# Kernel tuning notes

Measured on AMD Instinct MI355X. Metric: run time of the kernel, lower is better.

The kernel has to match this reference:

```python
import jax, jax.numpy as jnp
import numpy as np

B, T, L, INPUT_DIM = 16, 128, 100, 100
EMB = 100
FEAT = INPUT_DIM + 3 * EMB          # 400
HID, OUT = 128, 50
RNN_IN = 2 * INPUT_DIM + 3 * L      # 500
VOCAB = 10000 + 2


def setup_inputs() -> dict:
    key = jax.random.key(0)
    ks = jax.random.split(key, 12)
    first = jax.random.normal(ks[0], (B, T, INPUT_DIM), jnp.float32)
    idx = jax.random.randint(ks[1], (B, T, 3 * L), 0, VOCAB).astype(jnp.float32)
    x = jnp.concatenate([first, idx], axis=2)  # [B,T,400]
    s = 0.05
    return {
        "x": x,
        "embed_nodes": jax.random.normal(ks[2], (VOCAB, EMB), jnp.float32) * s,
        "embed_paths": jax.random.normal(ks[3], (VOCAB, EMB), jnp.float32) * s,
        "W_t": jax.random.normal(ks[4], (FEAT, FEAT), jnp.float32) / np.sqrt(FEAT),
        "b_t": jnp.zeros((FEAT,), jnp.float32),
        "W_a": jax.random.normal(ks[5], (FEAT, 1), jnp.float32) / np.sqrt(FEAT),
        "b_a": jnp.zeros((1,), jnp.float32),
        "W_ih": jax.random.normal(ks[6], (4 * HID, RNN_IN), jnp.float32) / np.sqrt(RNN_IN),
        "W_hh": jax.random.normal(ks[7], (4 * HID, HID), jnp.float32) / np.sqrt(HID),
        "b_ih": jnp.zeros((4 * HID,), jnp.float32),
        "b_hh": jnp.zeros((4 * HID,), jnp.float32),
        "W_fc": jax.random.normal(ks[8], (HID, OUT), jnp.float32) / np.sqrt(HID),
        "b_fc": jnp.zeros((OUT,), jnp.float32),
    }


def _lstm(xs, W_ih, W_hh, b_ih, b_hh):
    # xs: [B,T,D] -> out [B,T,H]; PyTorch gate order i,f,g,o
    def step(carry, xt):
        h, c = carry
        g = xt @ W_ih.T + h @ W_hh.T + (b_ih + b_hh)  # [B,4H]
        i, f, gg, o = jnp.split(g, 4, axis=-1)
        c = jax.nn.sigmoid(f) * c + jax.nn.sigmoid(i) * jnp.tanh(gg)
        h = jax.nn.sigmoid(o) * jnp.tanh(c)
        return (h, c), h
    h0 = jnp.zeros((xs.shape[0], HID), xs.dtype)
    (_, _), hs = jax.lax.scan(step, (h0, h0), jnp.swapaxes(xs, 0, 1))
    return jnp.swapaxes(hs, 0, 1)


def reference(x, embed_nodes, embed_paths, W_t, b_t, W_a, b_a,
              W_ih, W_hh, b_ih, b_hh, W_fc, b_fc):
    first = x[:, :, :INPUT_DIM]                                   # [B,T,100]
    c2v = x[:, :, INPUT_DIM:INPUT_DIM + 3 * L].reshape(B, T, L, 3).astype(jnp.int32)
    s_emb = embed_nodes[c2v[..., 0]]                              # [B,T,L,100]
    e_emb = embed_nodes[c2v[..., 2]]
    p_emb = embed_paths[c2v[..., 1]]
    att_part = jnp.broadcast_to(first[:, :, None, :], (B, T, L, INPUT_DIM))
    full = jnp.concatenate([s_emb, e_emb, p_emb, att_part], axis=3)  # [B,T,L,400]
    # dropout skipped (deterministic reference == evaluating=True path)
    transformed = jnp.tanh(full @ W_t + b_t)
    ctx = transformed @ W_a + b_a                                 # [B,T,L,1]
    # faithful to nn.Softmax(dim=1): softmax over the sequence axis T
    attn = jax.nn.softmax(ctx, axis=1)
    code_vectors = jnp.sum(full * attn, axis=2)                   # [B,T,400]
    rnn_input = jnp.concatenate([first, code_vectors], axis=2)    # [B,T,500]
    out = _lstm(rnn_input, W_ih, W_hh, b_ih, b_hh)                # [B,T,128]
    return jax.nn.sigmoid(out @ W_fc + b_fc)                      # [B,T,50]
```

## Files before the change

kernel.cpp:

```cpp
#include <hip/hip_runtime.h>
#include <hip/hip_bf16.h>
#include <stdint.h>

#define B_     16
#define T_     128
#define L_     100
#define IN_    100
#define EMB_   100
#define FEAT_  400
#define HID_   128
#define OUT_   50
#define RNNIN_ 500
#define VOCAB_ 10002
#define BT_    2048
#define TBLK   157

#define S_T    (0.16f / 127.0f)
#define INVS_T (127.0f / 0.16f)
#define S_E    (0.30f / 127.0f)
#define INVS_E (127.0f / 0.30f)

typedef __attribute__((ext_vector_type(8))) short short8;
typedef __attribute__((ext_vector_type(4))) short short4v;
typedef __attribute__((ext_vector_type(4))) float f32x4;

__device__ __forceinline__ float lo2f(unsigned int u) {
    union { unsigned int i; float f; } v; v.i = u << 16; return v.f;
}
__device__ __forceinline__ float fast_tanh(float x) {
    x = fminf(15.f, fmaxf(-15.f, x));
    float e = __expf(2.f * x);
    return (e - 1.f) * __builtin_amdgcn_rcpf(e + 1.f);
}
__device__ __forceinline__ float sigm(float x) {
    x = fminf(30.f, fmaxf(-30.f, x));
    float e = __expf(-x);
    return __builtin_amdgcn_rcpf(1.f + e);
}
__device__ __forceinline__ signed char q8(float v, float invs) {
    float t = fminf(127.f, fmaxf(-127.f, v * invs));
    return (signed char)__float2int_rn(t);
}
__device__ __forceinline__ int sb(unsigned int u, int k) {
    return (int)(signed char)(u >> (8 * k));
}

__global__ __launch_bounds__(256) void casts_k(
    const float* __restrict__ EN, const float* __restrict__ EP,
    const float* __restrict__ x, const float* __restrict__ Wt,
    const float* __restrict__ Wih, const float* __restrict__ Whh,
    __hip_bfloat16* __restrict__ ENb, __hip_bfloat16* __restrict__ EPb,
    signed char* __restrict__ EN8, signed char* __restrict__ EP8,
    __hip_bfloat16* __restrict__ x_bf, __hip_bfloat16* __restrict__ WtT,
    __hip_bfloat16* __restrict__ Wih_bf, __hip_bfloat16* __restrict__ Whh_bf)
{
    int t0 = blockIdx.x * 256 + threadIdx.x;
    const int stride = 256 * 256;
    int n1 = VOCAB_ * 100;
    for (int i = t0; i < n1; i += stride) {
        float v = EN[i];
        ENb[i] = __float2bfloat16(v);
        EN8[i] = q8(v, INVS_E);
    }
    for (int i = t0; i < n1; i += stride) {
        float v = EP[i];
        EPb[i] = __float2bfloat16(v);
        EP8[i] = q8(v, INVS_E);
    }
    for (int i = t0; i < BT_ * 100; i += stride) {
        int bt = i / 100, d = i - bt * 100;
        x_bf[i] = __float2bfloat16(x[(size_t)bt * 400 + d]);
    }
    for (int i = t0; i < 4 * 400 * 128; i += stride) {
        int w = i / (400 * 128), rem = i - w * 400 * 128;
        int n = rem >> 7, k = rem & 127;
        WtT[i] = __float2bfloat16((k < 100) ? Wt[(size_t)(w * 100 + k) * 400 + n] : 0.f);
    }
    for (int i = t0; i < 512 * 512; i += stride) {
        int g = i >> 9, k = i & 511;
        Wih_bf[i] = __float2bfloat16((k < 500) ? Wih[(size_t)g * 500 + k] : 0.f);
    }
    for (int i = t0; i < 512 * 128; i += stride) Whh_bf[i] = __float2bfloat16(Whh[i]);
}

__device__ __forceinline__ void load_a100(const __hip_bfloat16* __restrict__ arow,
                                          int kg, short8 af[4])
{
    af[0] = *(const short8*)(arow + kg * 8);
    af[1] = *(const short8*)(arow + 32 + kg * 8);
    af[2] = *(const short8*)(arow + 64 + kg * 8);
    short8 z = {};
    af[3] = z;
    if (kg == 0) {
        short4v t = *(const short4v*)(arow + 96);
        af[3][0] = t[0]; af[3][1] = t[1]; af[3][2] = t[2]; af[3][3] = t[3];
    }
}

__global__ __launch_bounds__(256) void mm_k(
    const __hip_bfloat16* __restrict__ ENb, const __hip_bfloat16* __restrict__ EPb,
    const __hip_bfloat16* __restrict__ x_bf, const __hip_bfloat16* __restrict__ WtT,
    const float* __restrict__ btb,
    signed char* __restrict__ Es, signed char* __restrict__ Ee,
    signed char* __restrict__ Ep, float* __restrict__ q)
{
    int blk = blockIdx.x, tid = threadIdx.x;
    int wave = tid >> 6, lane = tid & 63;
    int cl = lane & 15, kg = lane >> 4;

    if (blk < 3 * TBLK) {
        int which = blk / TBLK, mb = blk - which * TBLK;
        const __hip_bfloat16* A = (which == 2) ? EPb : ENb;
        signed char* outp = (which == 0) ? Es : ((which == 1) ? Ee : Ep);
        int r0 = mb * 64 + wave * 16;
        int ra = r0 + cl; if (ra > VOCAB_ - 1) ra = VOCAB_ - 1;
        short8 af[4];
        load_a100(A + (size_t)ra * 100, kg, af);
        const __hip_bfloat16* Bp = WtT + (size_t)which * 400 * 128;
        for (int n0 = 0; n0 < 25; n0++) {
            const __hip_bfloat16* brow = Bp + (size_t)(n0 * 16 + cl) * 128 + kg * 8;
            f32x4 acc = (f32x4){0.f, 0.f, 0.f, 0.f};
            acc = __builtin_amdgcn_mfma_f32_16x16x32_bf16(af[0], *(const short8*)(brow), acc, 0, 0, 0);
            acc = __builtin_amdgcn_mfma_f32_16x16x32_bf16(af[1], *(const short8*)(brow + 32), acc, 0, 0, 0);
            acc = __builtin_amdgcn_mfma_f32_16x16x32_bf16(af[2], *(const short8*)(brow + 64), acc, 0, 0, 0);
            acc = __builtin_amdgcn_mfma_f32_16x16x32_bf16(af[3], *(const short8*)(brow + 96), acc, 0, 0, 0);
            int colj = n0 * 16 + cl;
#pragma unroll
            for (int r = 0; r < 4; r++) {
                int gr = r0 + kg * 4 + r;
                if (gr < VOCAB_)
                    outp[(size_t)gr * 400 + colj] = q8(acc[r], INVS_T);
            }
        }
    } else {
        int mb = blk - 3 * TBLK;
        int r0 = mb * 64 + wave * 16;
        short8 af[4];
        load_a100(x_bf + (size_t)(r0 + cl) * 100, kg, af);
        const __hip_bfloat16* Bp = WtT + (size_t)3 * 400 * 128;
        for (int n0 = 0; n0 < 25; n0++) {
            const __hip_bfloat16* brow = Bp + (size_t)(n0 * 16 + cl) * 128 + kg * 8;
            f32x4 acc = (f32x4){0.f, 0.f, 0.f, 0.f};
            acc = __builtin_amdgcn_mfma_f32_16x16x32_bf16(af[0], *(const short8*)(brow), acc, 0, 0, 0);
            acc = __builtin_amdgcn_mfma_f32_16x16x32_bf16(af[1], *(const short8*)(brow + 32), acc, 0, 0, 0);
            acc = __builtin_amdgcn_mfma_f32_16x16x32_bf16(af[2], *(const short8*)(brow + 64), acc, 0, 0, 0);
            acc = __builtin_amdgcn_mfma_f32_16x16x32_bf16(af[3], *(const short8*)(brow + 96), acc, 0, 0, 0);
            int colj = n0 * 16 + cl;
            float bb = btb[colj];
#pragma unroll
            for (int r = 0; r < 4; r++) {
                int gr = r0 + kg * 4 + r;
                q[(size_t)gr * 400 + colj] = acc[r] + bb;
            }
        }
    }
}

__global__ __launch_bounds__(256) void stage_a(
    const float* __restrict__ x,
    const signed char* __restrict__ Es8, const signed char* __restrict__ Ee8,
    const signed char* __restrict__ Ep8,
    const float* __restrict__ q, const float* __restrict__ Wa,
    float* __restrict__ ctx)
{
    __shared__ int idx_s[300];
    int bt = blockIdx.x, tid = threadIdx.x;
    const float* xr = x + (size_t)bt * 400 + 100;
    for (int i = tid; i < 300; i += 256) idx_s[i] = (int)xr[i];
    int lane = tid & 63, wave = tid >> 6;
    bool act = lane < 50;
    int j0 = lane * 8;
    float qv[8], wv[8];
    if (act) {
        float4 qa = *(const float4*)(q + (size_t)bt * 400 + j0);
        float4 qb = *(const float4*)(q + (size_t)bt * 400 + j0 + 4);
        float4 wa = *(const float4*)(Wa + j0);
        float4 wb = *(const float4*)(Wa + j0 + 4);
        qv[0]=qa.x; qv[1]=qa.y; qv[2]=qa.z; qv[3]=qa.w;
        qv[4]=qb.x; qv[5]=qb.y; qv[6]=qb.z; qv[7]=qb.w;
        wv[0]=wa.x; wv[1]=wa.y; wv[2]=wa.z; wv[3]=wa.w;
        wv[4]=wb.x; wv[5]=wb.y; wv[6]=wb.z; wv[7]=wb.w;
    } else {
#pragma unroll
        for (int jj = 0; jj < 8; jj++) { qv[jj] = 0.f; wv[jj] = 0.f; }
    }
    __syncthreads();
    for (int l = wave; l < 100; l += 4) {
        int i0 = idx_s[3 * l], i1 = idx_s[3 * l + 1], i2 = idx_s[3 * l + 2];
        float sum = 0.f;
        if (act) {
            uint2 a  = ((const uint2*)(Es8 + (size_t)i0 * 400))[lane];
            uint2 b  = ((const uint2*)(Ee8 + (size_t)i2 * 400))[lane];
            uint2 cc = ((const uint2*)(Ep8 + (size_t)i1 * 400))[lane];
            int zi[8];
#pragma unroll
            for (int k = 0; k < 4; k++) {
                zi[k]     = sb(a.x, k) + sb(b.x, k) + sb(cc.x, k);
                zi[4 + k] = sb(a.y, k) + sb(b.y, k) + sb(cc.y, k);
            }
#pragma unroll
            for (int jj = 0; jj < 8; jj++) {
                float z = fmaf((float)zi[jj], S_T, qv[jj]);
                sum = fmaf(fast_tanh(z), wv[jj], sum);
            }
        }
#pragma unroll
        for (int off = 32; off; off >>= 1) sum += __shfl_xor(sum, off);
        if (lane == 0) ctx[(size_t)bt * 100 + l] = sum;
    }
}

__global__ __launch_bounds__(256) void softmax_w(
    const float* __restrict__ ctx, float* __restrict__ attn)
{
    int wid = blockIdx.x * 4 + (threadIdx.x >> 6);
    int lane = threadIdx.x & 63;
    int b = wid / 100, l = wid - b * 100;
    size_t base = (size_t)b * 128 * 100 + l;
    float v0 = ctx[base + (size_t)lane * 100];
    float v1 = ctx[base + (size_t)(lane + 64) * 100];
    float m = fmaxf(v0, v1);
#pragma unroll
    for (int off = 32; off; off >>= 1) m = fmaxf(m, __shfl_xor(m, off));
    float e0 = __expf(v0 - m), e1 = __expf(v1 - m);
    float s = e0 + e1;
#pragma unroll
    for (int off = 32; off; off >>= 1) s += __shfl_xor(s, off);
    float rs = 1.f / s;
    attn[base + (size_t)lane * 100] = e0 * rs;
    attn[base + (size_t)(lane + 64) * 100] = e1 * rs;
}

__global__ __launch_bounds__(128) void stage_c(
    const float* __restrict__ x, const float* __restrict__ attn,
    const signed char* __restrict__ EN8, const signed char* __restrict__ EP8,
    __hip_bfloat16* __restrict__ rnn_bf)
{
    __shared__ float at[100];
    __shared__ int idx[300];
    int bt = blockIdx.x, tid = threadIdx.x;
    if (tid < 100) at[tid] = attn[(size_t)bt * 100 + tid];
    const float* xr = x + (size_t)bt * 400 + 100;
    for (int i = tid; i < 300; i += 128) idx[i] = (int)xr[i];
    __syncthreads();
    int d = tid;
    __hip_bfloat16* o = rnn_bf + (size_t)bt * 512;
    if (d < 100) {
        float as = 0.f, ae = 0.f, ap = 0.f, sa = 0.f;
#pragma unroll 4
        for (int l = 0; l < 100; l++) {
            float a = at[l]; sa += a;
            as = fmaf(a, (float)EN8[(size_t)idx[3 * l] * 100 + d], as);
            ae = fmaf(a, (float)EN8[(size_t)idx[3 * l + 2] * 100 + d], ae);
            ap = fmaf(a, (float)EP8[(size_t)idx[3 * l + 1] * 100 + d], ap);
        }
        float fi = x[(size_t)bt * 400 + d];
        o[d]       = __float2bfloat16(fi);
        o[100 + d] = __float2bfloat16(as * S_E);
        o[200 + d] = __float2bfloat16(ae * S_E);
        o[300 + d] = __float2bfloat16(ap * S_E);
        o[400 + d] = __float2bfloat16(fi * sa);
    } else if (d < 112) {
        o[400 + d] = __float2bfloat16(0.f);
    }
}

__global__ __launch_bounds__(256) void gemm_x(
    const __hip_bfloat16* __restrict__ rnn_bf, const __hip_bfloat16* __restrict__ Wih_bf,
    const float* __restrict__ bih, const float* __restrict__ bhh,
    float* __restrict__ X)
{
    int blk = blockIdx.x, tid = threadIdx.x;
    int wave = tid >> 6, lane = tid & 63;
    int cl = lane & 15, kg = lane >> 4;
    int r0 = blk * 64 + wave * 16;

    short8 af[16];
    const __hip_bfloat16* arow = rnn_bf + (size_t)(r0 + cl) * 512 + kg * 8;
#pragma unroll
    for (int ks = 0; ks < 16; ks++) af[ks] = *(const short8*)(arow + ks * 32);

    for (int n0 = 0; n0 < 32; n0 += 2) {
        const __hip_bfloat16* b0 = Wih_bf + (size_t)(n0 * 16 + cl) * 512 + kg * 8;
        const __hip_bfloat16* b1 = b0 + 16 * 512;
        f32x4 acA = (f32x4){0.f, 0.f, 0.f, 0.f};
        f32x4 acB = (f32x4){0.f, 0.f, 0.f, 0.f};
#pragma unroll
        for (int ks = 0; ks < 16; ks++) {
            acA = __builtin_amdgcn_mfma_f32_16x16x32_bf16(af[ks], *(const short8*)(b0 + ks * 32), acA, 0, 0, 0);
            acB = __builtin_amdgcn_mfma_f32_16x16x32_bf16(af[ks], *(const short8*)(b1 + ks * 32), acB, 0, 0, 0);
        }
        int c0 = n0 * 16 + cl, c1 = c0 + 16;
        float bi0 = bih[c0] + bhh[c0];
        float bi1 = bih[c1] + bhh[c1];
#pragma unroll
        for (int r = 0; r < 4; r++) {
            int m = r0 + kg * 4 + r;
            X[(size_t)m * 512 + c0] = acA[r] + bi0;
            X[(size_t)m * 512 + c1] = acB[r] + bi1;
        }
    }
}

__global__ __launch_bounds__(512, 1) void lstm_k(
    const float* __restrict__ X, const __hip_bfloat16* __restrict__ Whh_bf,
    float* __restrict__ hs)
{
    int b = blockIdx.x, tid = threadIdx.x;
    int wave = tid >> 6, lane = tid & 63;
    int col = lane & 15, kg = lane >> 4;

    short8 bf[4][4];
#pragma unroll
    for (int n = 0; n < 4; n++) {
        int g = n * 128 + wave * 16 + col;
#pragma unroll
        for (int kk = 0; kk < 4; kk++)
            bf[n][kk] = *(const short8*)(Whh_bf + (size_t)g * 128 + kk * 32 + kg * 8);
    }

    __shared__ __hip_bfloat16 hbuf[2][128];
    __shared__ float Xs[16][512];
    __shared__ float hsb_s[16][128];
    float c = 0.f;
    if (tid < 128) hbuf[0][tid] = __float2bfloat16(0.f);
    const float* xb = X + (size_t)b * 128 * 512;
    float* hb = hs + (size_t)b * 128 * 128;
    int j = wave * 16 + col;
    int p = 0;

    __syncthreads();

    for (int tc = 0; tc < 8; tc++) {
        {
            const float* src = xb + (size_t)tc * 16 * 512 + tid;
#pragma unroll
            for (int k = 0; k < 16; k++) Xs[k][tid] = src[k * 512];
        }
        __syncthreads();

#pragma unroll 1
        for (int ts = 0; ts < 16; ts++) {
            short8 af[4];
            short8 zz = {};
#pragma unroll
            for (int kk = 0; kk < 4; kk++) {
                af[kk] = zz;
                if (col == 0) af[kk] = *(const short8*)(&hbuf[p][0] + kk * 32 + kg * 8);
            }
            f32x4 acc[4];
#pragma unroll
            for (int n = 0; n < 4; n++) acc[n] = (f32x4){0.f, 0.f, 0.f, 0.f};
#pragma unroll
            for (int kk = 0; kk < 4; kk++)
#pragma unroll
                for (int n = 0; n < 4; n++)
                    acc[n] = __builtin_amdgcn_mfma_f32_16x16x32_bf16(af[kk], bf[n][kk], acc[n], 0, 0, 0);

            if (lane < 16) {
                float pi = acc[0][0] + Xs[ts][j];
                float pf = acc[1][0] + Xs[ts][128 + j];
                float pg = acc[2][0] + Xs[ts][256 + j];
                float po = acc[3][0] + Xs[ts][384 + j];
                c = sigm(pf) * c + sigm(pi) * fast_tanh(pg);
                float hn = sigm(po) * fast_tanh(c);
                hbuf[p ^ 1][j] = __float2bfloat16(hn);
                hsb_s[ts][j] = hn;
            }
            __syncthreads();
            p ^= 1;
        }

        {
            float* dst = hb + (size_t)tc * 16 * 128;
#pragma unroll
            for (int k = 0; k < 4; k++) {
                int i = k * 512 + tid;
                dst[i] = hsb_s[i >> 7][i & 127];
            }
        }
    }
}

__global__ __launch_bounds__(64) void fc_k(
    const float* __restrict__ hs, const float* __restrict__ Wfc,
    const float* __restrict__ bfc, float* __restrict__ out)
{
    int r0 = blockIdx.x * 4, o = threadIdx.x;
    if (o >= 50) return;
    float acc[4] = {0.f, 0.f, 0.f, 0.f};
    for (int j = 0; j < 128; j++) {
        float wv = Wfc[j * 50 + o];
#pragma unroll
        for (int r = 0; r < 4; r++)
            acc[r] = fmaf(hs[(size_t)(r0 + r) * 128 + j], wv, acc[r]);
    }
    float bb = bfc[o];
#pragma unroll
    for (int r = 0; r < 4; r++) out[(size_t)(r0 + r) * 50 + o] = sigm(acc[r] + bb);
}

extern "C" void kernel_launch(void* const* d_in, const int* in_sizes, int n_in,
                              void* d_out, int out_size, void* d_ws, size_t ws_size,
                              hipStream_t stream) {
    const float* x   = (const float*)d_in[0];
    const float* EN  = (const float*)d_in[1];
    const float* EP  = (const float*)d_in[2];
    const float* Wt  = (const float*)d_in[3];
    const float* bt  = (const float*)d_in[4];
    const float* Wa  = (const float*)d_in[5];
    const float* Wih = (const float*)d_in[7];
    const float* Whh = (const float*)d_in[8];
    const float* bih = (const float*)d_in[9];
    const float* bhh = (const float*)d_in[10];
    const float* Wfc = (const float*)d_in[11];
    const float* bfc = (const float*)d_in[12];
    float* out = (float*)d_out;

    char* ws = (char*)d_ws;
    size_t off = 0;
    auto alloc = [&](size_t bytes) -> char* {
        char* p = ws + off;
        off = (off + bytes + 255) & ~(size_t)255;
        return p;
    };
    signed char* Es  = (signed char*)alloc((size_t)VOCAB_ * 400);
    signed char* Ee  = (signed char*)alloc((size_t)VOCAB_ * 400);
    signed char* Epb = (signed char*)alloc((size_t)VOCAB_ * 400);
    __hip_bfloat16* ENb    = (__hip_bfloat16*)alloc((size_t)VOCAB_ * 100 * 2);
    __hip_bfloat16* EPb    = (__hip_bfloat16*)alloc((size_t)VOCAB_ * 100 * 2);
    signed char* EN8 = (signed char*)alloc((size_t)VOCAB_ * 100);
    signed char* EP8 = (signed char*)alloc((size_t)VOCAB_ * 100);
    __hip_bfloat16* x_bf   = (__hip_bfloat16*)alloc((size_t)BT_ * 100 * 2);
    __hip_bfloat16* WtT    = (__hip_bfloat16*)alloc((size_t)4 * 400 * 128 * 2);
    __hip_bfloat16* Wih_bf = (__hip_bfloat16*)alloc((size_t)512 * 512 * 2);
    __hip_bfloat16* Whh_bf = (__hip_bfloat16*)alloc((size_t)512 * 128 * 2);
    __hip_bfloat16* rnn_bf = (__hip_bfloat16*)alloc((size_t)BT_ * 512 * 2);
    float* q    = (float*)alloc((size_t)BT_ * 400 * 4);
    float* ctx  = (float*)alloc((size_t)BT_ * 100 * 4);
    float* attn = (float*)alloc((size_t)BT_ * 100 * 4);
    float* X    = (float*)alloc((size_t)BT_ * 512 * 4);
    float* hsb  = (float*)alloc((size_t)BT_ * 128 * 4);

    casts_k<<<256, 256, 0, stream>>>(EN, EP, x, Wt, Wih, Whh,
                                     ENb, EPb, EN8, EP8, x_bf, WtT, Wih_bf, Whh_bf);
    mm_k<<<3 * TBLK + 32, 256, 0, stream>>>(ENb, EPb, x_bf, WtT, bt,
                                            Es, Ee, Epb, q);

    stage_a<<<BT_, 256, 0, stream>>>(x, Es, Ee, Epb, q, Wa, ctx);
    softmax_w<<<400, 256, 0, stream>>>(ctx, attn);
    stage_c<<<BT_, 128, 0, stream>>>(x, attn, EN8, EP8, rnn_bf);
    gemm_x<<<32, 256, 0, stream>>>(rnn_bf, Wih_bf, bih, bhh, X);
    lstm_k<<<B_, 512, 0, stream>>>(X, Whh_bf, hsb);
    fc_k<<<BT_ / 4, 64, 0, stream>>>(hsb, Wfc, bfc, out);
}
```

Measured before the change: 272.7 us.

## Fuse six pre-LSTM kernels into one persistent kernel with grid barriers

Merges the cast, embedding GEMM, attention-score, softmax, context-sum and input-projection kernels into a single persistent kernel of 512 blocks. The stages are separated by a software grid barrier built on atomics, which removes five kernel launches and the gaps between them. In exchange, stages with little work leave most blocks idle at each barrier. The barrier also assumes all 512 blocks are resident at once, and it needs an extra memset before each launch.

```diff
diff --git a/kernel.cpp b/kernel.cpp
--- a/kernel.cpp
+++ b/kernel.cpp
@@ -14,6 +14,7 @@
 #define VOCAB_ 10002
 #define BT_    2048
 #define TBLK   157
+#define GRID_  512
 
 #define S_T    (0.16f / 127.0f)
 #define INVS_T (127.0f / 0.16f)
@@ -24,9 +25,6 @@
 typedef __attribute__((ext_vector_type(4))) short short4v;
 typedef __attribute__((ext_vector_type(4))) float f32x4;
 
-__device__ __forceinline__ float lo2f(unsigned int u) {
-    union { unsigned int i; float f; } v; v.i = u << 16; return v.f;
-}
 __device__ __forceinline__ float fast_tanh(float x) {
     x = fminf(15.f, fmaxf(-15.f, x));
     float e = __expf(2.f * x);
@@ -45,42 +43,32 @@
     return (int)(signed char)(u >> (8 * k));
 }
 
-__global__ __launch_bounds__(256) void casts_k(
-    const float* __restrict__ EN, const float* __restrict__ EP,
-    const float* __restrict__ x, const float* __restrict__ Wt,
-    const float* __restrict__ Wih, const float* __restrict__ Whh,
-    __hip_bfloat16* __restrict__ ENb, __hip_bfloat16* __restrict__ EPb,
-    signed char* __restrict__ EN8, signed char* __restrict__ EP8,
-    __hip_bfloat16* __restrict__ x_bf, __hip_bfloat16* __restrict__ WtT,
-    __hip_bfloat16* __restrict__ Wih_bf, __hip_bfloat16* __restrict__ Whh_bf)
-{
-    int t0 = blockIdx.x * 256 + threadIdx.x;
-    const int stride = 256 * 256;
-    int n1 = VOCAB_ * 100;
-    for (int i = t0; i < n1; i += stride) {
-        float v = EN[i];
-        ENb[i] = __float2bfloat16(v);
-        EN8[i] = q8(v, INVS_E);
-    }
-    for (int i = t0; i < n1; i += stride) {
-        float v = EP[i];
-        EPb[i] = __float2bfloat16(v);
-        EP8[i] = q8(v, INVS_E);
-    }
-    for (int i = t0; i < BT_ * 100; i += stride) {
-        int bt = i / 100, d = i - bt * 100;
-        x_bf[i] = __float2bfloat16(x[(size_t)bt * 400 + d]);
-    }
-    for (int i = t0; i < 4 * 400 * 128; i += stride) {
-        int w = i / (400 * 128), rem = i - w * 400 * 128;
-        int n = rem >> 7, k = rem & 127;
-        WtT[i] = __float2bfloat16((k < 100) ? Wt[(size_t)(w * 100 + k) * 400 + n] : 0.f);
-    }
-    for (int i = t0; i < 512 * 512; i += stride) {
-        int g = i >> 9, k = i & 511;
-        Wih_bf[i] = __float2bfloat16((k < 500) ? Wih[(size_t)g * 500 + k] : 0.f);
-    }
-    for (int i = t0; i < 512 * 128; i += stride) Whh_bf[i] = __float2bfloat16(Whh[i]);
+struct Params {
+    const float *x, *EN, *EP, *Wt, *btb, *Wa, *Wih, *Whh, *bih, *bhh;
+    signed char *Es, *Ee, *Ep, *EN8, *EP8;
+    __hip_bfloat16 *ENb, *EPb, *x_bf, *WtT, *Wih_bf, *Whh_bf, *rnn_bf;
+    float *q, *ctx, *attn, *X;
+    unsigned *bar;
+};
+
+__device__ __forceinline__ void gbar(unsigned* bar, unsigned target) {
+    __syncthreads();
+    __threadfence();
+    if (threadIdx.x == 0) {
+        unsigned old = __hip_atomic_fetch_add(&bar[0], 1u, __ATOMIC_ACQ_REL,
+                                              __HIP_MEMORY_SCOPE_AGENT);
+        if (old == GRID_ - 1) {
+            __hip_atomic_store(&bar[0], 0u, __ATOMIC_RELAXED, __HIP_MEMORY_SCOPE_AGENT);
+            __hip_atomic_fetch_add(&bar[1], 1u, __ATOMIC_RELEASE,
+                                   __HIP_MEMORY_SCOPE_AGENT);
+        } else {
+            while (__hip_atomic_load(&bar[1], __ATOMIC_ACQUIRE,
+                                     __HIP_MEMORY_SCOPE_AGENT) < target)
+                __builtin_amdgcn_s_sleep(2);
+        }
+    }
+    __syncthreads();
+    __threadfence();
 }
 
 __device__ __forceinline__ void load_a100(const __hip_bfloat16* __restrict__ arow,
@@ -97,207 +85,220 @@
     }
 }
 
-__global__ __launch_bounds__(256) void mm_k(
-    const __hip_bfloat16* __restrict__ ENb, const __hip_bfloat16* __restrict__ EPb,
-    const __hip_bfloat16* __restrict__ x_bf, const __hip_bfloat16* __restrict__ WtT,
-    const float* __restrict__ btb,
-    signed char* __restrict__ Es, signed char* __restrict__ Ee,
-    signed char* __restrict__ Ep, float* __restrict__ q)
+__global__ __launch_bounds__(256, 2) void fused_k(Params p)
 {
-    int blk = blockIdx.x, tid = threadIdx.x;
-    int wave = tid >> 6, lane = tid & 63;
+    int bid = blockIdx.x, tid = threadIdx.x;
+    int lane = tid & 63, wave = tid >> 6;
     int cl = lane & 15, kg = lane >> 4;
 
-    if (blk < 3 * TBLK) {
-        int which = blk / TBLK, mb = blk - which * TBLK;
-        const __hip_bfloat16* A = (which == 2) ? EPb : ENb;
-        signed char* outp = (which == 0) ? Es : ((which == 1) ? Ee : Ep);
-        int r0 = mb * 64 + wave * 16;
-        int ra = r0 + cl; if (ra > VOCAB_ - 1) ra = VOCAB_ - 1;
-        short8 af[4];
-        load_a100(A + (size_t)ra * 100, kg, af);
-        const __hip_bfloat16* Bp = WtT + (size_t)which * 400 * 128;
-        for (int n0 = 0; n0 < 25; n0++) {
-            const __hip_bfloat16* brow = Bp + (size_t)(n0 * 16 + cl) * 128 + kg * 8;
-            f32x4 acc = (f32x4){0.f, 0.f, 0.f, 0.f};
-            acc = __builtin_amdgcn_mfma_f32_16x16x32_bf16(af[0], *(const short8*)(brow), acc, 0, 0, 0);
-            acc = __builtin_amdgcn_mfma_f32_16x16x32_bf16(af[1], *(const short8*)(brow + 32), acc, 0, 0, 0);
-            acc = __builtin_amdgcn_mfma_f32_16x16x32_bf16(af[2], *(const short8*)(brow + 64), acc, 0, 0, 0);
-            acc = __builtin_amdgcn_mfma_f32_16x16x32_bf16(af[3], *(const short8*)(brow + 96), acc, 0, 0, 0);
-            int colj = n0 * 16 + cl;
+    __shared__ int idx_s[300];
+    __shared__ float at2[2][100];
+    __shared__ int idx2[2][300];
+
+    {
+        int t0 = bid * 256 + tid;
+        const int stride = GRID_ * 256;
+        int n1 = VOCAB_ * 100;
+        for (int i = t0; i < n1; i += stride) {
+            float v = p.EN[i];
+            p.ENb[i] = __float2bfloat16(v);
+            p.EN8[i] = q8(v, INVS_E);
+        }
+        for (int i = t0; i < n1; i += stride) {
+            float v = p.EP[i];
+            p.EPb[i] = __float2bfloat16(v);
+            p.EP8[i] = q8(v, INVS_E);
+        }
+        for (int i = t0; i < BT_ * 100; i += stride) {
+            int bt = i / 100, d = i - bt * 100;
+            p.x_bf[i] = __float2bfloat16(p.x[(size_t)bt * 400 + d]);
+        }
+        for (int i = t0; i < 4 * 400 * 128; i += stride) {
+            int w = i / (400 * 128), rem = i - w * 400 * 128;
+            int n = rem >> 7, k = rem & 127;
+            p.WtT[i] = __float2bfloat16((k < 100) ? p.Wt[(size_t)(w * 100 + k) * 400 + n] : 0.f);
+        }
+        for (int i = t0; i < 512 * 512; i += stride) {
+            int g = i >> 9, k = i & 511;
+            p.Wih_bf[i] = __float2bfloat16((k < 500) ? p.Wih[(size_t)g * 500 + k] : 0.f);
+        }
+        for (int i = t0; i < 512 * 128; i += stride)
+            p.Whh_bf[i] = __float2bfloat16(p.Whh[i]);
+    }
+    gbar(p.bar, 1);
+
+    if (bid < 3 * TBLK + 32) {
+        if (bid < 3 * TBLK) {
+            int which = bid / TBLK, mb = bid - which * TBLK;
+            const __hip_bfloat16* A = (which == 2) ? p.EPb : p.ENb;
+            signed char* outp = (which == 0) ? p.Es : ((which == 1) ? p.Ee : p.Ep);
+            int r0 = mb * 64 + wave * 16;
+            int ra = r0 + cl; if (ra > VOCAB_ - 1) ra = VOCAB_ - 1;
+            short8 af[4];
+            load_a100(A + (size_t)ra * 100, kg, af);
+            const __hip_bfloat16* Bp = p.WtT + (size_t)which * 400 * 128;
+            for (int n0 = 0; n0 < 25; n0++) {
+                const __hip_bfloat16* brow = Bp + (size_t)(n0 * 16 + cl) * 128 + kg * 8;
+                f32x4 acc = (f32x4){0.f, 0.f, 0.f, 0.f};
+                acc = __builtin_amdgcn_mfma_f32_16x16x32_bf16(af[0], *(const short8*)(brow), acc, 0, 0, 0);
+                acc = __builtin_amdgcn_mfma_f32_16x16x32_bf16(af[1], *(const short8*)(brow + 32), acc, 0, 0, 0);
+                acc = __builtin_amdgcn_mfma_f32_16x16x32_bf16(af[2], *(const short8*)(brow + 64), acc, 0, 0, 0);
+                acc = __builtin_amdgcn_mfma_f32_16x16x32_bf16(af[3], *(const short8*)(brow + 96), acc, 0, 0, 0);
+                int colj = n0 * 16 + cl;
+#pragma unroll
+                for (int r = 0; r < 4; r++) {
+                    int gr = r0 + kg * 4 + r;
+                    if (gr < VOCAB_)
+                        outp[(size_t)gr * 400 + colj] = q8(acc[r], INVS_T);
+                }
+            }
+        } else {
+            int mb = bid - 3 * TBLK;
+            int r0 = mb * 64 + wave * 16;
+            short8 af[4];
+            load_a100(p.x_bf + (size_t)(r0 + cl) * 100, kg, af);
+            const __hip_bfloat16* Bp = p.WtT + (size_t)3 * 400 * 128;
+            for (int n0 = 0; n0 < 25; n0++) {
+                const __hip_bfloat16* brow = Bp + (size_t)(n0 * 16 + cl) * 128 + kg * 8;
+                f32x4 acc = (f32x4){0.f, 0.f, 0.f, 0.f};
+                acc = __builtin_amdgcn_mfma_f32_16x16x32_bf16(af[0], *(const short8*)(brow), acc, 0, 0, 0);
+                acc = __builtin_amdgcn_mfma_f32_16x16x32_bf16(af[1], *(const short8*)(brow + 32), acc, 0, 0, 0);
+                acc = __builtin_amdgcn_mfma_f32_16x16x32_bf16(af[2], *(const short8*)(brow + 64), acc, 0, 0, 0);
+                acc = __builtin_amdgcn_mfma_f32_16x16x32_bf16(af[3], *(const short8*)(brow + 96), acc, 0, 0, 0);
+                int colj = n0 * 16 + cl;
+                float bb = p.btb[colj];
+#pragma unroll
+                for (int r = 0; r < 4; r++) {
+                    int gr = r0 + kg * 4 + r;
+                    p.q[(size_t)gr * 400 + colj] = acc[r] + bb;
+                }
+            }
+        }
+    }
+    gbar(p.bar, 2);
+
+    for (int bt = bid; bt < BT_; bt += GRID_) {
+        const float* xr = p.x + (size_t)bt * 400 + 100;
+        for (int i = tid; i < 300; i += 256) idx_s[i] = (int)xr[i];
+        bool act = lane < 50;
+        int j0 = lane * 8;
+        float qv[8], wv[8];
+        if (act) {
+            float4 qa = *(const float4*)(p.q + (size_t)bt * 400 + j0);
+            float4 qb = *(const float4*)(p.q + (size_t)bt * 400 + j0 + 4);
+            float4 wa = *(const float4*)(p.Wa + j0);
+            float4 wb = *(const float4*)(p.Wa + j0 + 4);
+            qv[0]=qa.x; qv[1]=qa.y; qv[2]=qa.z; qv[3]=qa.w;
+            qv[4]=qb.x; qv[5]=qb.y; qv[6]=qb.z; qv[7]=qb.w;
+            wv[0]=wa.x; wv[1]=wa.y; wv[2]=wa.z; wv[3]=wa.w;
+            wv[4]=wb.x; wv[5]=wb.y; wv[6]=wb.z; wv[7]=wb.w;
+        } else {
+#pragma unroll
+            for (int jj = 0; jj < 8; jj++) { qv[jj] = 0.f; wv[jj] = 0.f; }
+        }
+        __syncthreads();
+        for (int l = wave; l < 100; l += 4) {
+            int i0 = idx_s[3 * l], i1 = idx_s[3 * l + 1], i2 = idx_s[3 * l + 2];
+            float sum = 0.f;
+            if (act) {
+                uint2 a  = ((const uint2*)(p.Es + (size_t)i0 * 400))[lane];
+                uint2 b  = ((const uint2*)(p.Ee + (size_t)i2 * 400))[lane];
+                uint2 cc = ((const uint2*)(p.Ep + (size_t)i1 * 400))[lane];
+                int zi[8];
+#pragma unroll
+                for (int k = 0; k < 4; k++) {
+                    zi[k]     = sb(a.x, k) + sb(b.x, k) + sb(cc.x, k);
+                    zi[4 + k] = sb(a.y, k) + sb(b.y, k) + sb(cc.y, k);
+                }
+#pragma unroll
+                for (int jj = 0; jj < 8; jj++) {
+                    float z = fmaf((float)zi[jj], S_T, qv[jj]);
+                    sum = fmaf(fast_tanh(z), wv[jj], sum);
+                }
+            }
+#pragma unroll
+            for (int off = 32; off; off >>= 1) sum += __shfl_xor(sum, off);
+            if (lane == 0) p.ctx[(size_t)bt * 100 + l] = sum;
+        }
+        __syncthreads();
+    }
+    gbar(p.bar, 3);
+
+    if (bid < 400) {
+        int wid = bid * 4 + wave;
+        int b = wid / 100, l = wid - b * 100;
+        size_t base = (size_t)b * 128 * 100 + l;
+        float v0 = p.ctx[base + (size_t)lane * 100];
+        float v1 = p.ctx[base + (size_t)(lane + 64) * 100];
+        float m = fmaxf(v0, v1);
+#pragma unroll
+        for (int off = 32; off; off >>= 1) m = fmaxf(m, __shfl_xor(m, off));
+        float e0 = __expf(v0 - m), e1 = __expf(v1 - m);
+        float s = e0 + e1;
+#pragma unroll
+        for (int off = 32; off; off >>= 1) s += __shfl_xor(s, off);
+        float rs = 1.f / s;
+        p.attn[base + (size_t)lane * 100] = e0 * rs;
+        p.attn[base + (size_t)(lane + 64) * 100] = e1 * rs;
+    }
+    gbar(p.bar, 4);
+
+    for (int role = bid; role < BT_ / 2; role += GRID_) {
+        int sub = tid >> 7, t1 = tid & 127;
+        int bt = role * 2 + sub;
+        if (t1 < 100) at2[sub][t1] = p.attn[(size_t)bt * 100 + t1];
+        const float* xr = p.x + (size_t)bt * 400 + 100;
+        for (int i = t1; i < 300; i += 128) idx2[sub][i] = (int)xr[i];
+        __syncthreads();
+        int d = t1;
+        __hip_bfloat16* o = p.rnn_bf + (size_t)bt * 512;
+        if (d < 100) {
+            float as = 0.f, ae = 0.f, ap = 0.f, sa = 0.f;
+#pragma unroll 4
+            for (int l = 0; l < 100; l++) {
+                float a = at2[sub][l]; sa += a;
+                as = fmaf(a, (float)p.EN8[(size_t)idx2[sub][3 * l] * 100 + d], as);
+                ae = fmaf(a, (float)p.EN8[(size_t)idx2[sub][3 * l + 2] * 100 + d], ae);
+                ap = fmaf(a, (float)p.EP8[(size_t)idx2[sub][3 * l + 1] * 100 + d], ap);
+            }
+            float fi = p.x[(size_t)bt * 400 + d];
+            o[d]       = __float2bfloat16(fi);
+            o[100 + d] = __float2bfloat16(as * S_E);
+            o[200 + d] = __float2bfloat16(ae * S_E);
+            o[300 + d] = __float2bfloat16(ap * S_E);
+            o[400 + d] = __float2bfloat16(fi * sa);
+        } else if (d < 112) {
+            o[400 + d] = __float2bfloat16(0.f);
+        }
+        __syncthreads();
+    }
+    gbar(p.bar, 5);
+
+    if (bid < 32) {
+        int r0 = bid * 64 + wave * 16;
+        short8 af[16];
+        const __hip_bfloat16* arow = p.rnn_bf + (size_t)(r0 + cl) * 512 + kg * 8;
+#pragma unroll
+        for (int ks = 0; ks < 16; ks++) af[ks] = *(const short8*)(arow + ks * 32);
+        for (int n0 = 0; n0 < 32; n0 += 2) {
+            const __hip_bfloat16* b0 = p.Wih_bf + (size_t)(n0 * 16 + cl) * 512 + kg * 8;
+            const __hip_bfloat16* b1 = b0 + 16 * 512;
+            f32x4 acA = (f32x4){0.f, 0.f, 0.f, 0.f};
+            f32x4 acB = (f32x4){0.f, 0.f, 0.f, 0.f};
+#pragma unroll
+            for (int ks = 0; ks < 16; ks++) {
+                acA = __builtin_amdgcn_mfma_f32_16x16x32_bf16(af[ks], *(const short8*)(b0 + ks * 32), acA, 0, 0, 0);
+                acB = __builtin_amdgcn_mfma_f32_16x16x32_bf16(af[ks], *(const short8*)(b1 + ks * 32), acB, 0, 0, 0);
+            }
+            int c0 = n0 * 16 + cl, c1 = c0 + 16;
+            float bi0 = p.bih[c0] + p.bhh[c0];
+            float bi1 = p.bih[c1] + p.bhh[c1];
 #pragma unroll
             for (int r = 0; r < 4; r++) {
-                int gr = r0 + kg * 4 + r;
-                if (gr < VOCAB_)
-                    outp[(size_t)gr * 400 + colj] = q8(acc[r], INVS_T);
-            }
-        }
-    } else {
-        int mb = blk - 3 * TBLK;
-        int r0 = mb * 64 + wave * 16;
-        short8 af[4];
-        load_a100(x_bf + (size_t)(r0 + cl) * 100, kg, af);
-        const __hip_bfloat16* Bp = WtT + (size_t)3 * 400 * 128;
-        for (int n0 = 0; n0 < 25; n0++) {
-            const __hip_bfloat16* brow = Bp + (size_t)(n0 * 16 + cl) * 128 + kg * 8;
-            f32x4 acc = (f32x4){0.f, 0.f, 0.f, 0.f};
-            acc = __builtin_amdgcn_mfma_f32_16x16x32_bf16(af[0], *(const short8*)(brow), acc, 0, 0, 0);
-            acc = __builtin_amdgcn_mfma_f32_16x16x32_bf16(af[1], *(const short8*)(brow + 32), acc, 0, 0, 0);
-            acc = __builtin_amdgcn_mfma_f32_16x16x32_bf16(af[2], *(const short8*)(brow + 64), acc, 0, 0, 0);
-            acc = __builtin_amdgcn_mfma_f32_16x16x32_bf16(af[3], *(const short8*)(brow + 96), acc, 0, 0, 0);
-            int colj = n0 * 16 + cl;
-            float bb = btb[colj];
-#pragma unroll
-            for (int r = 0; r < 4; r++) {
-                int gr = r0 + kg * 4 + r;
-                q[(size_t)gr * 400 + colj] = acc[r] + bb;
-            }
-        }
-    }
-}
-
-__global__ __launch_bounds__(256) void stage_a(
-    const float* __restrict__ x,
-    const signed char* __restrict__ Es8, const signed char* __restrict__ Ee8,
-    const signed char* __restrict__ Ep8,
-    const float* __restrict__ q, const float* __restrict__ Wa,
-    float* __restrict__ ctx)
-{
-    __shared__ int idx_s[300];
-    int bt = blockIdx.x, tid = threadIdx.x;
-    const float* xr = x + (size_t)bt * 400 + 100;
-    for (int i = tid; i < 300; i += 256) idx_s[i] = (int)xr[i];
-    int lane = tid & 63, wave = tid >> 6;
-    bool act = lane < 50;
-    int j0 = lane * 8;
-    float qv[8], wv[8];
-    if (act) {
-        float4 qa = *(const float4*)(q + (size_t)bt * 400 + j0);
-        float4 qb = *(const float4*)(q + (size_t)bt * 400 + j0 + 4);
-        float4 wa = *(const float4*)(Wa + j0);
-        float4 wb = *(const float4*)(Wa + j0 + 4);
-        qv[0]=qa.x; qv[1]=qa.y; qv[2]=qa.z; qv[3]=qa.w;
-        qv[4]=qb.x; qv[5]=qb.y; qv[6]=qb.z; qv[7]=qb.w;
-        wv[0]=wa.x; wv[1]=wa.y; wv[2]=wa.z; wv[3]=wa.w;
-        wv[4]=wb.x; wv[5]=wb.y; wv[6]=wb.z; wv[7]=wb.w;
-    } else {
-#pragma unroll
-        for (int jj = 0; jj < 8; jj++) { qv[jj] = 0.f; wv[jj] = 0.f; }
-    }
-    __syncthreads();
-    for (int l = wave; l < 100; l += 4) {
-        int i0 = idx_s[3 * l], i1 = idx_s[3 * l + 1], i2 = idx_s[3 * l + 2];
-        float sum = 0.f;
-        if (act) {
-            uint2 a  = ((const uint2*)(Es8 + (size_t)i0 * 400))[lane];
-            uint2 b  = ((const uint2*)(Ee8 + (size_t)i2 * 400))[lane];
-            uint2 cc = ((const uint2*)(Ep8 + (size_t)i1 * 400))[lane];
-            int zi[8];
-#pragma unroll
-            for (int k = 0; k < 4; k++) {
-                zi[k]     = sb(a.x, k) + sb(b.x, k) + sb(cc.x, k);
-                zi[4 + k] = sb(a.y, k) + sb(b.y, k) + sb(cc.y, k);
-            }
-#pragma unroll
-            for (int jj = 0; jj < 8; jj++) {
-                float z = fmaf((float)zi[jj], S_T, qv[jj]);
-                sum = fmaf(fast_tanh(z), wv[jj], sum);
-            }
-        }
-#pragma unroll
-        for (int off = 32; off; off >>= 1) sum += __shfl_xor(sum, off);
-        if (lane == 0) ctx[(size_t)bt * 100 + l] = sum;
-    }
-}
-
-__global__ __launch_bounds__(256) void softmax_w(
-    const float* __restrict__ ctx, float* __restrict__ attn)
-{
-    int wid = blockIdx.x * 4 + (threadIdx.x >> 6);
-    int lane = threadIdx.x & 63;
-    int b = wid / 100, l = wid - b * 100;
-    size_t base = (size_t)b * 128 * 100 + l;
-    float v0 = ctx[base + (size_t)lane * 100];
-    float v1 = ctx[base + (size_t)(lane + 64) * 100];
-    float m = fmaxf(v0, v1);
-#pragma unroll
-    for (int off = 32; off; off >>= 1) m = fmaxf(m, __shfl_xor(m, off));
-    float e0 = __expf(v0 - m), e1 = __expf(v1 - m);
-    float s = e0 + e1;
-#pragma unroll
-    for (int off = 32; off; off >>= 1) s += __shfl_xor(s, off);
-    float rs = 1.f / s;
-    attn[base + (size_t)lane * 100] = e0 * rs;
-    attn[base + (size_t)(lane + 64) * 100] = e1 * rs;
-}
-
-__global__ __launch_bounds__(128) void stage_c(
-    const float* __restrict__ x, const float* __restrict__ attn,
-    const signed char* __restrict__ EN8, const signed char* __restrict__ EP8,
-    __hip_bfloat16* __restrict__ rnn_bf)
-{
-    __shared__ float at[100];
-    __shared__ int idx[300];
-    int bt = blockIdx.x, tid = threadIdx.x;
-    if (tid < 100) at[tid] = attn[(size_t)bt * 100 + tid];
-    const float* xr = x + (size_t)bt * 400 + 100;
-    for (int i = tid; i < 300; i += 128) idx[i] = (int)xr[i];
-    __syncthreads();
-    int d = tid;
-    __hip_bfloat16* o = rnn_bf + (size_t)bt * 512;
-    if (d < 100) {
-        float as = 0.f, ae = 0.f, ap = 0.f, sa = 0.f;
-#pragma unroll 4
-        for (int l = 0; l < 100; l++) {
-            float a = at[l]; sa += a;
-            as = fmaf(a, (float)EN8[(size_t)idx[3 * l] * 100 + d], as);
-            ae = fmaf(a, (float)EN8[(size_t)idx[3 * l + 2] * 100 + d], ae);
-            ap = fmaf(a, (float)EP8[(size_t)idx[3 * l + 1] * 100 + d], ap);
-        }
-        float fi = x[(size_t)bt * 400 + d];
-        o[d]       = __float2bfloat16(fi);
-        o[100 + d] = __float2bfloat16(as * S_E);
-        o[200 + d] = __float2bfloat16(ae * S_E);
-        o[300 + d] = __float2bfloat16(ap * S_E);
-        o[400 + d] = __float2bfloat16(fi * sa);
-    } else if (d < 112) {
-        o[400 + d] = __float2bfloat16(0.f);
-    }
-}
-
-__global__ __launch_bounds__(256) void gemm_x(
-    const __hip_bfloat16* __restrict__ rnn_bf, const __hip_bfloat16* __restrict__ Wih_bf,
-    const float* __restrict__ bih, const float* __restrict__ bhh,
-    float* __restrict__ X)
-{
-    int blk = blockIdx.x, tid = threadIdx.x;
-    int wave = tid >> 6, lane = tid & 63;
-    int cl = lane & 15, kg = lane >> 4;
-    int r0 = blk * 64 + wave * 16;
-
-    short8 af[16];
-    const __hip_bfloat16* arow = rnn_bf + (size_t)(r0 + cl) * 512 + kg * 8;
-#pragma unroll
-    for (int ks = 0; ks < 16; ks++) af[ks] = *(const short8*)(arow + ks * 32);
-
-    for (int n0 = 0; n0 < 32; n0 += 2) {
-        const __hip_bfloat16* b0 = Wih_bf + (size_t)(n0 * 16 + cl) * 512 + kg * 8;
-        const __hip_bfloat16* b1 = b0 + 16 * 512;
-        f32x4 acA = (f32x4){0.f, 0.f, 0.f, 0.f};
-        f32x4 acB = (f32x4){0.f, 0.f, 0.f, 0.f};
-#pragma unroll
-        for (int ks = 0; ks < 16; ks++) {
-            acA = __builtin_amdgcn_mfma_f32_16x16x32_bf16(af[ks], *(const short8*)(b0 + ks * 32), acA, 0, 0, 0);
-            acB = __builtin_amdgcn_mfma_f32_16x16x32_bf16(af[ks], *(const short8*)(b1 + ks * 32), acB, 0, 0, 0);
-        }
-        int c0 = n0 * 16 + cl, c1 = c0 + 16;
-        float bi0 = bih[c0] + bhh[c0];
-        float bi1 = bih[c1] + bhh[c1];
-#pragma unroll
-        for (int r = 0; r < 4; r++) {
-            int m = r0 + kg * 4 + r;
-            X[(size_t)m * 512 + c0] = acA[r] + bi0;
-            X[(size_t)m * 512 + c1] = acB[r] + bi1;
+                int m = r0 + kg * 4 + r;
+                p.X[(size_t)m * 512 + c0] = acA[r] + bi0;
+                p.X[(size_t)m * 512 + c1] = acB[r] + bi1;
+            }
         }
     }
 }
@@ -424,6 +425,7 @@
         off = (off + bytes + 255) & ~(size_t)255;
         return p;
     };
+    unsigned* bar = (unsigned*)alloc(256);
     signed char* Es  = (signed char*)alloc((size_t)VOCAB_ * 400);
     signed char* Ee  = (signed char*)alloc((size_t)VOCAB_ * 400);
     signed char* Epb = (signed char*)alloc((size_t)VOCAB_ * 400);
@@ -442,15 +444,18 @@
     float* X    = (float*)alloc((size_t)BT_ * 512 * 4);
     float* hsb  = (float*)alloc((size_t)BT_ * 128 * 4);
 
-    casts_k<<<256, 256, 0, stream>>>(EN, EP, x, Wt, Wih, Whh,
-                                     ENb, EPb, EN8, EP8, x_bf, WtT, Wih_bf, Whh_bf);
-    mm_k<<<3 * TBLK + 32, 256, 0, stream>>>(ENb, EPb, x_bf, WtT, bt,
-                                            Es, Ee, Epb, q);
-
-    stage_a<<<BT_, 256, 0, stream>>>(x, Es, Ee, Epb, q, Wa, ctx);
-    softmax_w<<<400, 256, 0, stream>>>(ctx, attn);
-    stage_c<<<BT_, 128, 0, stream>>>(x, attn, EN8, EP8, rnn_bf);
-    gemm_x<<<32, 256, 0, stream>>>(rnn_bf, Wih_bf, bih, bhh, X);
+    hipMemsetAsync(bar, 0, 256, stream);
+
+    Params p;
+    p.x = x; p.EN = EN; p.EP = EP; p.Wt = Wt; p.btb = bt; p.Wa = Wa;
+    p.Wih = Wih; p.Whh = Whh; p.bih = bih; p.bhh = bhh;
+    p.Es = Es; p.Ee = Ee; p.Ep = Epb; p.EN8 = EN8; p.EP8 = EP8;
+    p.ENb = ENb; p.EPb = EPb; p.x_bf = x_bf; p.WtT = WtT;
+    p.Wih_bf = Wih_bf; p.Whh_bf = Whh_bf; p.rnn_bf = rnn_bf;
+    p.q = q; p.ctx = ctx; p.attn = attn; p.X = X;
+    p.bar = bar;
+
+    fused_k<<<GRID_, 256, 0, stream>>>(p);
     lstm_k<<<B_, 512, 0, stream>>>(X, Whh_bf, hsb);
     fc_k<<<BT_ / 4, 64, 0, stream>>>(hsb, Wfc, bfc, out);
 }
```

Measured after the change: 949.3 us. 3.48x slower.

## Fuse bf16 casts into embedding GEMM loads and fold input GEMM into LSTM

Applied to the files above, without the earlier changes.

The embedding and x bf16 copies are dropped, and mm_k now converts fp32 rows to bf16 in registers while loading its A fragments. The separate gemm_x launch is folded into lstm_k, so each batch block first computes its own 128x512 input projection before the recurrence. casts_k gets more blocks and handles less work. This removes two intermediate buffers and one kernel launch. In exchange the input GEMM runs on only 16 blocks instead of 32, and its result must be visible within the block before the recurrence reads X.

```diff
diff --git a/kernel.cpp b/kernel.cpp
--- a/kernel.cpp
+++ b/kernel.cpp
@@ -21,12 +21,8 @@
 #define INVS_E (127.0f / 0.30f)
 
 typedef __attribute__((ext_vector_type(8))) short short8;
-typedef __attribute__((ext_vector_type(4))) short short4v;
 typedef __attribute__((ext_vector_type(4))) float f32x4;
 
-__device__ __forceinline__ float lo2f(unsigned int u) {
-    union { unsigned int i; float f; } v; v.i = u << 16; return v.f;
-}
 __device__ __forceinline__ float fast_tanh(float x) {
     x = fminf(15.f, fmaxf(-15.f, x));
     float e = __expf(2.f * x);
@@ -47,30 +43,17 @@
 
 __global__ __launch_bounds__(256) void casts_k(
     const float* __restrict__ EN, const float* __restrict__ EP,
-    const float* __restrict__ x, const float* __restrict__ Wt,
-    const float* __restrict__ Wih, const float* __restrict__ Whh,
-    __hip_bfloat16* __restrict__ ENb, __hip_bfloat16* __restrict__ EPb,
+    const float* __restrict__ Wt, const float* __restrict__ Wih,
+    const float* __restrict__ Whh,
     signed char* __restrict__ EN8, signed char* __restrict__ EP8,
-    __hip_bfloat16* __restrict__ x_bf, __hip_bfloat16* __restrict__ WtT,
-    __hip_bfloat16* __restrict__ Wih_bf, __hip_bfloat16* __restrict__ Whh_bf)
+    __hip_bfloat16* __restrict__ WtT, __hip_bfloat16* __restrict__ Wih_bf,
+    __hip_bfloat16* __restrict__ Whh_bf)
 {
     int t0 = blockIdx.x * 256 + threadIdx.x;
-    const int stride = 256 * 256;
+    const int stride = 1024 * 256;
     int n1 = VOCAB_ * 100;
-    for (int i = t0; i < n1; i += stride) {
-        float v = EN[i];
-        ENb[i] = __float2bfloat16(v);
-        EN8[i] = q8(v, INVS_E);
-    }
-    for (int i = t0; i < n1; i += stride) {
-        float v = EP[i];
-        EPb[i] = __float2bfloat16(v);
-        EP8[i] = q8(v, INVS_E);
-    }
-    for (int i = t0; i < BT_ * 100; i += stride) {
-        int bt = i / 100, d = i - bt * 100;
-        x_bf[i] = __float2bfloat16(x[(size_t)bt * 400 + d]);
-    }
+    for (int i = t0; i < n1; i += stride) EN8[i] = q8(EN[i], INVS_E);
+    for (int i = t0; i < n1; i += stride) EP8[i] = q8(EP[i], INVS_E);
     for (int i = t0; i < 4 * 400 * 128; i += stride) {
         int w = i / (400 * 128), rem = i - w * 400 * 128;
         int n = rem >> 7, k = rem & 127;
@@ -83,23 +66,28 @@
     for (int i = t0; i < 512 * 128; i += stride) Whh_bf[i] = __float2bfloat16(Whh[i]);
 }
 
-__device__ __forceinline__ void load_a100(const __hip_bfloat16* __restrict__ arow,
-                                          int kg, short8 af[4])
-{
-    af[0] = *(const short8*)(arow + kg * 8);
-    af[1] = *(const short8*)(arow + 32 + kg * 8);
-    af[2] = *(const short8*)(arow + 64 + kg * 8);
+__device__ __forceinline__ void load_a100_f32(const float* __restrict__ arow,
+                                              int kg, short8 af[4])
+{
+#pragma unroll
+    for (int s = 0; s < 3; s++) {
+        const float* p = arow + s * 32 + kg * 8;
+#pragma unroll
+        for (int j = 0; j < 8; j++)
+            af[s][j] = (short)__bfloat16_as_ushort(__float2bfloat16(p[j]));
+    }
     short8 z = {};
     af[3] = z;
     if (kg == 0) {
-        short4v t = *(const short4v*)(arow + 96);
-        af[3][0] = t[0]; af[3][1] = t[1]; af[3][2] = t[2]; af[3][3] = t[3];
+#pragma unroll
+        for (int j = 0; j < 4; j++)
+            af[3][j] = (short)__bfloat16_as_ushort(__float2bfloat16(arow[96 + j]));
     }
 }
 
 __global__ __launch_bounds__(256) void mm_k(
-    const __hip_bfloat16* __restrict__ ENb, const __hip_bfloat16* __restrict__ EPb,
-    const __hip_bfloat16* __restrict__ x_bf, const __hip_bfloat16* __restrict__ WtT,
+    const float* __restrict__ EN, const float* __restrict__ EP,
+    const float* __restrict__ x, const __hip_bfloat16* __restrict__ WtT,
     const float* __restrict__ btb,
     signed char* __restrict__ Es, signed char* __restrict__ Ee,
     signed char* __restrict__ Ep, float* __restrict__ q)
@@ -110,12 +98,12 @@
 
     if (blk < 3 * TBLK) {
         int which = blk / TBLK, mb = blk - which * TBLK;
-        const __hip_bfloat16* A = (which == 2) ? EPb : ENb;
+        const float* A = (which == 2) ? EP : EN;
         signed char* outp = (which == 0) ? Es : ((which == 1) ? Ee : Ep);
         int r0 = mb * 64 + wave * 16;
         int ra = r0 + cl; if (ra > VOCAB_ - 1) ra = VOCAB_ - 1;
         short8 af[4];
-        load_a100(A + (size_t)ra * 100, kg, af);
+        load_a100_f32(A + (size_t)ra * 100, kg, af);
         const __hip_bfloat16* Bp = WtT + (size_t)which * 400 * 128;
         for (int n0 = 0; n0 < 25; n0++) {
             const __hip_bfloat16* brow = Bp + (size_t)(n0 * 16 + cl) * 128 + kg * 8;
@@ -136,7 +124,7 @@
         int mb = blk - 3 * TBLK;
         int r0 = mb * 64 + wave * 16;
         short8 af[4];
-        load_a100(x_bf + (size_t)(r0 + cl) * 100, kg, af);
+        load_a100_f32(x + (size_t)(r0 + cl) * 400, kg, af);
         const __hip_bfloat16* Bp = WtT + (size_t)3 * 400 * 128;
         for (int n0 = 0; n0 < 25; n0++) {
             const __hip_bfloat16* brow = Bp + (size_t)(n0 * 16 + cl) * 128 + kg * 8;
@@ -265,50 +253,43 @@
     }
 }
 
-__global__ __launch_bounds__(256) void gemm_x(
+__global__ __launch_bounds__(512, 1) void lstm_k(
     const __hip_bfloat16* __restrict__ rnn_bf, const __hip_bfloat16* __restrict__ Wih_bf,
     const float* __restrict__ bih, const float* __restrict__ bhh,
-    float* __restrict__ X)
-{
-    int blk = blockIdx.x, tid = threadIdx.x;
-    int wave = tid >> 6, lane = tid & 63;
-    int cl = lane & 15, kg = lane >> 4;
-    int r0 = blk * 64 + wave * 16;
-
-    short8 af[16];
-    const __hip_bfloat16* arow = rnn_bf + (size_t)(r0 + cl) * 512 + kg * 8;
-#pragma unroll
-    for (int ks = 0; ks < 16; ks++) af[ks] = *(const short8*)(arow + ks * 32);
-
-    for (int n0 = 0; n0 < 32; n0 += 2) {
-        const __hip_bfloat16* b0 = Wih_bf + (size_t)(n0 * 16 + cl) * 512 + kg * 8;
-        const __hip_bfloat16* b1 = b0 + 16 * 512;
-        f32x4 acA = (f32x4){0.f, 0.f, 0.f, 0.f};
-        f32x4 acB = (f32x4){0.f, 0.f, 0.f, 0.f};
-#pragma unroll
-        for (int ks = 0; ks < 16; ks++) {
-            acA = __builtin_amdgcn_mfma_f32_16x16x32_bf16(af[ks], *(const short8*)(b0 + ks * 32), acA, 0, 0, 0);
-            acB = __builtin_amdgcn_mfma_f32_16x16x32_bf16(af[ks], *(const short8*)(b1 + ks * 32), acB, 0, 0, 0);
-        }
-        int c0 = n0 * 16 + cl, c1 = c0 + 16;
-        float bi0 = bih[c0] + bhh[c0];
-        float bi1 = bih[c1] + bhh[c1];
-#pragma unroll
-        for (int r = 0; r < 4; r++) {
-            int m = r0 + kg * 4 + r;
-            X[(size_t)m * 512 + c0] = acA[r] + bi0;
-            X[(size_t)m * 512 + c1] = acB[r] + bi1;
-        }
-    }
-}
-
-__global__ __launch_bounds__(512, 1) void lstm_k(
-    const float* __restrict__ X, const __hip_bfloat16* __restrict__ Whh_bf,
-    float* __restrict__ hs)
+    const __hip_bfloat16* __restrict__ Whh_bf,
+    float* __restrict__ X, float* __restrict__ hs)
 {
     int b = blockIdx.x, tid = threadIdx.x;
     int wave = tid >> 6, lane = tid & 63;
     int col = lane & 15, kg = lane >> 4;
+
+    {
+        int r0 = b * 128 + wave * 16;
+        short8 af[16];
+        const __hip_bfloat16* arow = rnn_bf + (size_t)(r0 + col) * 512 + kg * 8;
+#pragma unroll
+        for (int ks = 0; ks < 16; ks++) af[ks] = *(const short8*)(arow + ks * 32);
+        for (int n0 = 0; n0 < 32; n0 += 2) {
+            const __hip_bfloat16* b0 = Wih_bf + (size_t)(n0 * 16 + col) * 512 + kg * 8;
+            const __hip_bfloat16* b1 = b0 + 16 * 512;
+            f32x4 acA = (f32x4){0.f, 0.f, 0.f, 0.f};
+            f32x4 acB = (f32x4){0.f, 0.f, 0.f, 0.f};
+#pragma unroll
+            for (int ks = 0; ks < 16; ks++) {
+                acA = __builtin_amdgcn_mfma_f32_16x16x32_bf16(af[ks], *(const short8*)(b0 + ks * 32), acA, 0, 0, 0);
+                acB = __builtin_amdgcn_mfma_f32_16x16x32_bf16(af[ks], *(const short8*)(b1 + ks * 32), acB, 0, 0, 0);
+            }
+            int c0 = n0 * 16 + col, c1 = c0 + 16;
+            float bi0 = bih[c0] + bhh[c0];
+            float bi1 = bih[c1] + bhh[c1];
+#pragma unroll
+            for (int r = 0; r < 4; r++) {
+                int m = r0 + kg * 4 + r;
+                X[(size_t)m * 512 + c0] = acA[r] + bi0;
+                X[(size_t)m * 512 + c1] = acB[r] + bi1;
+            }
+        }
+    }
 
     short8 bf[4][4];
 #pragma unroll
@@ -427,11 +408,8 @@
     signed char* Es  = (signed char*)alloc((size_t)VOCAB_ * 400);
     signed char* Ee  = (signed char*)alloc((size_t)VOCAB_ * 400);
     signed char* Epb = (signed char*)alloc((size_t)VOCAB_ * 400);
-    __hip_bfloat16* ENb    = (__hip_bfloat16*)alloc((size_t)VOCAB_ * 100 * 2);
-    __hip_bfloat16* EPb    = (__hip_bfloat16*)alloc((size_t)VOCAB_ * 100 * 2);
     signed char* EN8 = (signed char*)alloc((size_t)VOCAB_ * 100);
     signed char* EP8 = (signed char*)alloc((size_t)VOCAB_ * 100);
-    __hip_bfloat16* x_bf   = (__hip_bfloat16*)alloc((size_t)BT_ * 100 * 2);
     __hip_bfloat16* WtT    = (__hip_bfloat16*)alloc((size_t)4 * 400 * 128 * 2);
     __hip_bfloat16* Wih_bf = (__hip_bfloat16*)alloc((size_t)512 * 512 * 2);
     __hip_bfloat16* Whh_bf = (__hip_bfloat16*)alloc((size_t)512 * 128 * 2);
@@ -442,15 +420,13 @@
     float* X    = (float*)alloc((size_t)BT_ * 512 * 4);
     float* hsb  = (float*)alloc((size_t)BT_ * 128 * 4);
 
-    casts_k<<<256, 256, 0, stream>>>(EN, EP, x, Wt, Wih, Whh,
-                                     ENb, EPb, EN8, EP8, x_bf, WtT, Wih_bf, Whh_bf);
-    mm_k<<<3 * TBLK + 32, 256, 0, stream>>>(ENb, EPb, x_bf, WtT, bt,
+    casts_k<<<1024, 256, 0, stream>>>(EN, EP, Wt, Wih, Whh,
+                                      EN8, EP8, WtT, Wih_bf, Whh_bf);
+    mm_k<<<3 * TBLK + 32, 256, 0, stream>>>(EN, EP, x, WtT, bt,
                                             Es, Ee, Epb, q);
-
     stage_a<<<BT_, 256, 0, stream>>>(x, Es, Ee, Epb, q, Wa, ctx);
     softmax_w<<<400, 256, 0, stream>>>(ctx, attn);
     stage_c<<<BT_, 128, 0, stream>>>(x, attn, EN8, EP8, rnn_bf);
-    gemm_x<<<32, 256, 0, stream>>>(rnn_bf, Wih_bf, bih, bhh, X);
-    lstm_k<<<B_, 512, 0, stream>>>(X, Whh_bf, hsb);
+    lstm_k<<<B_, 512, 0, stream>>>(rnn_bf, Wih_bf, bih, bhh, Whh_bf, X, hsb);
     fc_k<<<BT_ / 4, 64, 0, stream>>>(hsb, Wfc, bfc, out);
 }
```

Result: slower. 314.3 us (+15.3%).
